# Optimization experiments

Hardware: AMD Instinct MI355X
Metric: run time of the kernel (lower is better)

Reference implementation:

```python
import jax, jax.numpy as jnp
import numpy as np

NUM_SLOTS = 8
DIM = 256
ITERS = 3
EPS_LN = 1e-5

def _ln(x, g, b):
    mu = jnp.mean(x, axis=-1, keepdims=True)
    var = jnp.var(x, axis=-1, keepdims=True)
    return (x - mu) * jax.lax.rsqrt(var + EPS_LN) * g + b

def setup_inputs() -> dict:
    key = jax.random.key(0)
    ks = jax.random.split(key, 16)
    d = DIM
    s = 1.0 / np.sqrt(d)
    inp = {
        'x': jax.random.normal(ks[0], (64, 4096, d), jnp.float32),
        'noise': jax.random.normal(ks[1], (64, NUM_SLOTS, d), jnp.float32),
        'slots_mu': jax.random.normal(ks[2], (1, 1, d), jnp.float32),
        'slots_logsigma': jnp.zeros((1, 1, d), jnp.float32),
        'Wq': jax.random.uniform(ks[3], (d, d), jnp.float32, -s, s),
        'Wk': jax.random.uniform(ks[4], (d, d), jnp.float32, -s, s),
        'Wv': jax.random.uniform(ks[5], (d, d), jnp.float32, -s, s),
        'W_ih': jax.random.uniform(ks[6], (3 * d, d), jnp.float32, -s, s),
        'W_hh': jax.random.uniform(ks[7], (3 * d, d), jnp.float32, -s, s),
        'b_ih': jax.random.uniform(ks[8], (3 * d,), jnp.float32, -s, s),
        'b_hh': jax.random.uniform(ks[9], (3 * d,), jnp.float32, -s, s),
        'W1': jax.random.uniform(ks[10], (d, d), jnp.float32, -s, s),
        'b1': jax.random.uniform(ks[11], (d,), jnp.float32, -s, s),
        'W2': jax.random.uniform(ks[12], (d, d), jnp.float32, -s, s),
        'b2': jax.random.uniform(ks[13], (d,), jnp.float32, -s, s),
        'g_in': jnp.ones((d,), jnp.float32), 'be_in': jnp.zeros((d,), jnp.float32),
        'g_sl': jnp.ones((d,), jnp.float32), 'be_sl': jnp.zeros((d,), jnp.float32),
        'g_ff': jnp.ones((d,), jnp.float32), 'be_ff': jnp.zeros((d,), jnp.float32),
    }
    return inp

def _gru(x, h, W_ih, W_hh, b_ih, b_hh):
    # torch.nn.GRUCell math; x,h: [M, d]
    gi = x @ W_ih.T + b_ih
    gh = h @ W_hh.T + b_hh
    i_r, i_z, i_n = jnp.split(gi, 3, axis=-1)
    h_r, h_z, h_n = jnp.split(gh, 3, axis=-1)
    r = jax.nn.sigmoid(i_r + h_r)
    z = jax.nn.sigmoid(i_z + h_z)
    n = jnp.tanh(i_n + r * h_n)
    return (1.0 - z) * n + z * h

def reference(x, noise, slots_mu, slots_logsigma, Wq, Wk, Wv, W_ih, W_hh, b_ih, b_hh,
              W1, b1, W2, b2, g_in, be_in, g_sl, be_sl, g_ff, be_ff):
    B, N, d = x.shape
    scale = d ** (-0.5)
    x = _ln(x, g_in, be_in)
    slots = slots_mu + noise * jnp.exp(slots_logsigma)  # [B, K, d]
    # k/v are loop-invariant; hoist (same math as original)
    k = jnp.einsum('bnd,ed->bne', x, Wk)
    v = jnp.einsum('bnd,ed->bne', x, Wv)
    for _ in range(ITERS):
        slots_prev = slots
        q = jnp.einsum('bkd,ed->bke', _ln(slots, g_sl, be_sl), Wq)
        attn = jax.nn.softmax(jnp.einsum('bkd,bnd->bkn', q, k) * scale, axis=-1) + 1e-8
        attn = attn / jnp.sum(attn, axis=-1, keepdims=True)
        updates = jnp.einsum('bkn,bnd->bkd', attn, v)
        slots = _gru(updates.reshape(-1, d), slots_prev.reshape(-1, d),
                     W_ih, W_hh, b_ih, b_hh).reshape(B, NUM_SLOTS, d)
        h = jax.nn.relu(jnp.einsum('bkd,ed->bke', _ln(slots, g_ff, be_ff), W1) + b1)
        slots = slots + jnp.einsum('bkd,ed->bke', h, W2) + b2
    return slots.reshape(B, NUM_SLOTS * d)
```

## Files before the change

### kernel.cpp

```cpp
#include <hip/hip_runtime.h>
#include <cstddef>

#define DIM 256
#define NSLOT 8
#define BATCH 64
#define NTOK 4096
#define SEGB 16
#define NPART SEGB
#define ITERS 3
#define EPS 1e-5f

typedef short bf16x8 __attribute__((ext_vector_type(8)));
typedef short bf16x4 __attribute__((ext_vector_type(4)));
typedef float f32x4  __attribute__((ext_vector_type(4)));

static __device__ __forceinline__ short f2bf(float f) {
    union { float f; unsigned u; } v; v.f = f;
    unsigned r = v.u + 0x7fffu + ((v.u >> 16) & 1u);
    return (short)(r >> 16);
}

enum : size_t {
    OFF_M     = 0,
    OFF_WIHT  = OFF_M    + 256 * 256,
    OFF_WHHT  = OFF_WIHT + 256 * 768,
    OFF_WVT   = OFF_WHHT + 256 * 768,
    OFF_W1T   = OFF_WVT  + 256 * 256,
    OFF_W2T   = OFF_W1T  + 256 * 256,
    OFF_SLOTS = OFF_W2T  + 256 * 256,
    OFF_SNEW  = OFF_SLOTS + BATCH * NSLOT * 256,
    OFF_QT    = OFF_SNEW  + BATCH * NSLOT * 256,
    OFF_H     = OFF_QT    + BATCH * NSLOT * 256,
    OFF_UPD   = OFF_H     + BATCH * NSLOT * 256,
    OFF_UPART = OFF_UPD   + BATCH * NSLOT * 256,
    OFF_LPART = OFF_UPART + (size_t)BATCH * NPART * NSLOT * 256,
    WS_FLOATS = OFF_LPART + BATCH * NPART * 16
};

__global__ __launch_bounds__(256) void k_transpose(const float* __restrict__ w_ih,
                                                   const float* __restrict__ w_hh,
                                                   const float* __restrict__ wv,
                                                   const float* __restrict__ w1,
                                                   const float* __restrict__ w2,
                                                   float* __restrict__ ws) {
    int z = blockIdx.z;
    const float* src;
    float* dst;
    int R;
    if (z == 0)      { src = w_ih; dst = ws + OFF_WIHT; R = 768; }
    else if (z == 1) { src = w_hh; dst = ws + OFF_WHHT; R = 768; }
    else if (z == 2) { src = wv;   dst = ws + OFF_WVT;  R = 256; }
    else if (z == 3) { src = w1;   dst = ws + OFF_W1T;  R = 256; }
    else             { src = w2;   dst = ws + OFF_W2T;  R = 256; }
    if ((int)blockIdx.x * 32 >= R) return;
    __shared__ float tile[32][33];
    int lx = threadIdx.x & 31, ly = threadIdx.x >> 5;
    int r0 = blockIdx.x * 32, c0 = blockIdx.y * 32;
#pragma unroll
    for (int p = 0; p < 4; ++p)
        tile[ly + p * 8][lx] = src[(size_t)(r0 + ly + p * 8) * 256 + c0 + lx];
    __syncthreads();
#pragma unroll
    for (int p = 0; p < 4; ++p)
        dst[(size_t)(c0 + ly + p * 8) * R + r0 + lx] = tile[lx][ly + p * 8];
}

__global__ __launch_bounds__(256) void k_m(const float* __restrict__ wq,
                                           const float* __restrict__ wk,
                                           float* __restrict__ ws) {
    int d = blockIdx.x, t = threadIdx.x;
    float acc = 0.f;
    for (int e = 0; e < 256; ++e)
        acc += wq[e * 256 + d] * wk[e * 256 + t];
    ws[OFF_M + d * 256 + t] = acc * 0.0625f;
}

__global__ __launch_bounds__(256) void k_init(const float* __restrict__ mu,
                                              const float* __restrict__ logsig,
                                              const float* __restrict__ noise,
                                              float* __restrict__ ws) {
    int i = blockIdx.x * 256 + threadIdx.x;
    int d = i & 255;
    ws[OFF_SLOTS + i] = mu[d] + noise[i] * __expf(logsig[d]);
}

__global__ __launch_bounds__(256) void k_qt(float* __restrict__ ws,
                                            const float* __restrict__ g_sl,
                                            const float* __restrict__ be_sl) {
    __shared__ float ln[2048];
    int chunk = blockIdx.x, b = blockIdx.y;
    int t = threadIdx.x, wave = t >> 6, lane = t & 63;
    const float* slots = ws + OFF_SLOTS + b * 2048;
    float4 gf = ((const float4*)g_sl)[lane];
    float4 bf = ((const float4*)be_sl)[lane];
#pragma unroll
    for (int rr = 0; rr < 2; ++rr) {
        int r = wave + rr * 4;
        float4 v = ((const float4*)(slots + r * 256))[lane];
        float s1 = v.x + v.y + v.z + v.w;
        float s2 = v.x * v.x + v.y * v.y + v.z * v.z + v.w * v.w;
#pragma unroll
        for (int m = 1; m < 64; m <<= 1) { s1 += __shfl_xor(s1, m); s2 += __shfl_xor(s2, m); }
        float mu = s1 * (1.f / 256.f);
        float rstd = rsqrtf(s2 * (1.f / 256.f) - mu * mu + EPS);
        float4 o;
        o.x = (v.x - mu) * rstd * gf.x + bf.x;
        o.y = (v.y - mu) * rstd * gf.y + bf.y;
        o.z = (v.z - mu) * rstd * gf.z + bf.z;
        o.w = (v.w - mu) * rstd * gf.w + bf.w;
        *((float4*)&ln[r * 256 + lane * 4]) = o;
    }
    __syncthreads();
    const float* M = ws + OFF_M;
    int k0 = t >> 6;
    int e = chunk * 64 + (t & 63);
    float a0 = 0.f, a1 = 0.f;
    for (int d = 0; d < 256; ++d) {
        float m = M[d * 256 + e];
        a0 += ln[k0 * 256 + d] * m;
        a1 += ln[(k0 + 4) * 256 + d] * m;
    }
    float* qt = ws + OFF_QT + b * 2048;
    qt[k0 * 256 + e] = a0;
    qt[(k0 + 4) * 256 + e] = a1;
}

__global__ __launch_bounds__(256) void k_attn(const float* __restrict__ x,
                                              const float* __restrict__ g_in,
                                              const float* __restrict__ be_in,
                                              float* __restrict__ ws) {
    int seg = blockIdx.x, b = blockIdx.y;
    int t = threadIdx.x;
    int w = t >> 6, lane = t & 63;
    int q = lane >> 4, s16 = lane & 15;

    __shared__ short qhi[16 * 264];
    __shared__ short xT[256 * 64];
    __shared__ short Etmp[16 * 72];
    __shared__ float GsL[16], CsL[16];
    __shared__ float lsum[4][8], b1sLDS[4][8];

    const float* qtg = ws + OFF_QT + b * 2048;

    for (int idx = t; idx < 16 * 264; idx += 256) {
        int s = idx / 264, d = idx - s * 264;
        float v = (s < 8 && d < 256) ? qtg[s * 256 + d] * g_in[d] : 0.f;
        qhi[idx] = f2bf(v);
    }
    {
        if (t >= 8 && t < 16) { GsL[t] = 0.f; CsL[t] = 0.f; }
        int s = t >> 5, j = t & 31;
        float pg = 0.f, pc = 0.f;
        for (int d = j; d < 256; d += 32) {
            float qv = qtg[s * 256 + d];
            pg += qv * g_in[d];
            pc += qv * be_in[d];
        }
#pragma unroll
        for (int m = 1; m < 32; m <<= 1) { pg += __shfl_xor(pg, m); pc += __shfl_xor(pc, m); }
        if (j == 0) { GsL[s] = pg; CsL[s] = pc; }
    }
    __syncthreads();

    bf16x8 qf[8];
#pragma unroll
    for (int i = 0; i < 8; ++i)
        qf[i] = *(const bf16x8*)&qhi[s16 * 264 + i * 32 + q * 8];

    float Gv = GsL[s16], Cv = CsL[s16];

    f32x4 U[4];
#pragma unroll
    for (int c = 0; c < 4; ++c) U[c] = (f32x4){0.f, 0.f, 0.f, 0.f};
    float lacc = 0.f, b1acc = 0.f;

    const int tokens_per_block = NTOK / SEGB;
    const int tiles = tokens_per_block / 64;
    int mytok_base = seg * tokens_per_block + w * 16 + s16;
    int g0 = ((w * 16 + s16) >> 3);
    int t7 = s16 & 7;

    for (int tt = 0; tt < tiles; ++tt) {
        const float* xr = x + ((size_t)b * NTOK + (size_t)(mytok_base + tt * 64)) * 256 + q * 8;
        const float4* xp = (const float4*)xr;
        float4 xa[8], xb[8];
#pragma unroll
        for (int i = 0; i < 8; ++i) { xa[i] = xp[8 * i]; xb[i] = xp[8 * i + 1]; }
        float s1 = 0.f, s2 = 0.f;
#pragma unroll
        for (int i = 0; i < 8; ++i) {
            s1 += xa[i].x + xa[i].y + xa[i].z + xa[i].w + xb[i].x + xb[i].y + xb[i].z + xb[i].w;
            s2 += xa[i].x * xa[i].x + xa[i].y * xa[i].y + xa[i].z * xa[i].z + xa[i].w * xa[i].w
                + xb[i].x * xb[i].x + xb[i].y * xb[i].y + xb[i].z * xb[i].z + xb[i].w * xb[i].w;
        }
        s1 += __shfl_xor(s1, 16); s2 += __shfl_xor(s2, 16);
        s1 += __shfl_xor(s1, 32); s2 += __shfl_xor(s2, 32);
        float mu = s1 * (1.f / 256.f);
        float rstd = rsqrtf(s2 * (1.f / 256.f) - mu * mu + EPS);

        bf16x8 af[8];
#pragma unroll
        for (int i = 0; i < 8; ++i) {
            bf16x8 f;
            f[0] = f2bf(xa[i].x); f[1] = f2bf(xa[i].y); f[2] = f2bf(xa[i].z); f[3] = f2bf(xa[i].w);
            f[4] = f2bf(xb[i].x); f[5] = f2bf(xb[i].y); f[6] = f2bf(xb[i].z); f[7] = f2bf(xb[i].w);
            af[i] = f;
        }

        f32x4 Lc = (f32x4){0.f, 0.f, 0.f, 0.f};
#pragma unroll
        for (int i = 0; i < 8; ++i)
            Lc = __builtin_amdgcn_mfma_f32_16x16x32_bf16(af[i], qf[i], Lc, 0, 0, 0);

        float mur[4], rsr[4];
#pragma unroll
        for (int r = 0; r < 4; ++r) {
            mur[r] = __shfl(mu, q * 4 + r);
            rsr[r] = __shfl(rstd, q * 4 + r);
        }
        bf16x4 e2;
#pragma unroll
        for (int r = 0; r < 4; ++r) {
            float logit = rsr[r] * Lc[r] - mur[r] * rsr[r] * Gv + Cv;
            float E = __expf(fminf(logit, 30.f));
            lacc += E;
            b1acc += E * mur[r] * rsr[r];
            e2[r] = f2bf(E * rsr[r]);
        }

        __syncthreads();

#pragma unroll
        for (int i = 0; i < 8; ++i) {
            int Ki = (4 * i + q) & 7;
            int dbase = i * 32 + q * 8;
            bf16x8 f = af[i];
#pragma unroll
            for (int e = 0; e < 8; ++e) {
                int gp = (g0 ^ e ^ Ki) & 7;
                xT[((dbase + e) << 6) + (gp << 3) + t7] = f[e];
            }
        }
        *(bf16x4*)&Etmp[s16 * 72 + w * 16 + q * 4] = e2;

        __syncthreads();

        bf16x8 ea0 = *(const bf16x8*)&Etmp[s16 * 72 + q * 8];
        bf16x8 ea1 = *(const bf16x8*)&Etmp[s16 * 72 + 32 + q * 8];
#pragma unroll
        for (int c = 0; c < 4; ++c) {
            int d = (4 * w + c) * 16 + s16;
            int swz = (d ^ (d >> 3)) & 7;
            const short* row = &xT[d << 6];
            bf16x8 b0 = *(const bf16x8*)&row[((q ^ swz) & 7) << 3];
            bf16x8 b1 = *(const bf16x8*)&row[(((4 + q) ^ swz) & 7) << 3];
            U[c] = __builtin_amdgcn_mfma_f32_16x16x32_bf16(ea0, b0, U[c], 0, 0, 0);
            U[c] = __builtin_amdgcn_mfma_f32_16x16x32_bf16(ea1, b1, U[c], 0, 0, 0);
        }
    }

    lacc += __shfl_xor(lacc, 16); lacc += __shfl_xor(lacc, 32);
    b1acc += __shfl_xor(b1acc, 16); b1acc += __shfl_xor(b1acc, 32);
    __syncthreads();
    if (q == 0 && s16 < 8) { lsum[w][s16] = lacc; b1sLDS[w][s16] = b1acc; }
    __syncthreads();
    float* lpart = ws + OFF_LPART + (size_t)(b * NPART + seg) * 16;
    if (t < 8)  lpart[t] = lsum[0][t] + lsum[1][t] + lsum[2][t] + lsum[3][t];
    if (t >= 8 && t < 16) {
        int s = t - 8;
        lpart[8 + s] = b1sLDS[0][s] + b1sLDS[1][s] + b1sLDS[2][s] + b1sLDS[3][s];
    }
    float* up = ws + OFF_UPART + (size_t)(b * NPART + seg) * NSLOT * 256;
#pragma unroll
    for (int c = 0; c < 4; ++c) {
        int d = (4 * w + c) * 16 + s16;
#pragma unroll
        for (int r = 0; r < 4; ++r) {
            int slot = q * 4 + r;
            if (slot < 8) up[slot * 256 + d] = U[c][r];
        }
    }
}

__global__ __launch_bounds__(256) void k_upd(float* __restrict__ ws,
                                             const float* __restrict__ g_in,
                                             const float* __restrict__ be_in) {
    __shared__ float uc[2048];
    __shared__ float lsv[8], b1v[8];
    int b = blockIdx.x, t = threadIdx.x;
    if (t < 8) {
        float ls = 0.f, b1 = 0.f;
        for (int g = 0; g < NPART; ++g) {
            ls += ws[OFF_LPART + (size_t)(b * NPART + g) * 16 + t];
            b1 += ws[OFF_LPART + (size_t)(b * NPART + g) * 16 + 8 + t];
        }
        lsv[t] = ls; b1v[t] = b1;
    }
    float acc[8] = {0.f, 0.f, 0.f, 0.f, 0.f, 0.f, 0.f, 0.f};
    const float* up0 = ws + OFF_UPART + (size_t)b * NPART * 8 * 256;
    for (int g = 0; g < NPART; ++g) {
        const float* up = up0 + g * 2048;
#pragma unroll
        for (int s = 0; s < 8; ++s) acc[s] += up[s * 256 + t];
    }
    __syncthreads();
    float gd = g_in[t], bd = be_in[t];
#pragma unroll
    for (int s = 0; s < 8; ++s) {
        uc[s * 256 + t] = (gd * (acc[s] - b1v[s]) + bd * lsv[s]) / lsv[s];
    }
    __syncthreads();
    const float* WvT = ws + OFF_WVT;
    int k0 = t >> 6;
    int e0 = t & 63;
    float o0[4] = {0.f, 0.f, 0.f, 0.f};
    float o1[4] = {0.f, 0.f, 0.f, 0.f};
    for (int d = 0; d < 256; ++d) {
        float u0 = uc[k0 * 256 + d], u1 = uc[(k0 + 4) * 256 + d];
#pragma unroll
        for (int c = 0; c < 4; ++c) {
            float w = WvT[d * 256 + c * 64 + e0];
            o0[c] += u0 * w;
            o1[c] += u1 * w;
        }
    }
    float* updg = ws + OFF_UPD + b * 2048;
#pragma unroll
    for (int c = 0; c < 4; ++c) {
        updg[k0 * 256 + c * 64 + e0] = o0[c];
        updg[(k0 + 4) * 256 + c * 64 + e0] = o1[c];
    }
}

__global__ __launch_bounds__(256) void k_gru(float* __restrict__ ws,
                                             const float* __restrict__ b_ih,
                                             const float* __restrict__ b_hh) {
    __shared__ float upd[2048], sl[2048];
    int cg = blockIdx.x, b = blockIdx.y, t = threadIdx.x;
    const float* updg = ws + OFF_UPD + b * 2048;
    const float* slg = ws + OFF_SLOTS + b * 2048;
#pragma unroll
    for (int j = 0; j < 8; ++j) {
        upd[j * 256 + t] = updg[j * 256 + t];
        sl[j * 256 + t] = slg[j * 256 + t];
    }
    __syncthreads();
    int k = t >> 5, j = t & 31, c = cg * 32 + j;
    const float* WihT = ws + OFF_WIHT;
    const float* WhhT = ws + OFF_WHHT;
    float ar = 0.f, az = 0.f, an = 0.f, hr = 0.f, hz = 0.f, hn = 0.f;
    for (int d = 0; d < 256; ++d) {
        float ud = upd[k * 256 + d], sd = sl[k * 256 + d];
        const float* wi = WihT + d * 768;
        const float* wh = WhhT + d * 768;
        ar += ud * wi[c];       az += ud * wi[256 + c]; an += ud * wi[512 + c];
        hr += sd * wh[c];       hz += sd * wh[256 + c]; hn += sd * wh[512 + c];
    }
    float rg = 1.f / (1.f + __expf(-(ar + b_ih[c] + hr + b_hh[c])));
    float zg = 1.f / (1.f + __expf(-(az + b_ih[256 + c] + hz + b_hh[256 + c])));
    float ng = tanhf(an + b_ih[512 + c] + rg * (hn + b_hh[512 + c]));
    float hval = sl[k * 256 + c];
    ws[OFF_SNEW + b * 2048 + k * 256 + c] = (1.f - zg) * ng + zg * hval;
}

__global__ __launch_bounds__(256) void k_mlp1(float* __restrict__ ws,
                                              const float* __restrict__ g_ff,
                                              const float* __restrict__ be_ff,
                                              const float* __restrict__ b1v) {
    __shared__ float ln[2048];
    int chunk = blockIdx.x, b = blockIdx.y;
    int t = threadIdx.x, wave = t >> 6, lane = t & 63;
    const float* sn = ws + OFF_SNEW + b * 2048;
    float4 gf = ((const float4*)g_ff)[lane];
    float4 bf = ((const float4*)be_ff)[lane];
#pragma unroll
    for (int rr = 0; rr < 2; ++rr) {
        int r = wave + rr * 4;
        float4 v = ((const float4*)(sn + r * 256))[lane];
        float s1 = v.x + v.y + v.z + v.w;
        float s2 = v.x * v.x + v.y * v.y + v.z * v.z + v.w * v.w;
#pragma unroll
        for (int m = 1; m < 64; m <<= 1) { s1 += __shfl_xor(s1, m); s2 += __shfl_xor(s2, m); }
        float mu = s1 * (1.f / 256.f);
        float rstd = rsqrtf(s2 * (1.f / 256.f) - mu * mu + EPS);
        float4 o;
        o.x = (v.x - mu) * rstd * gf.x + bf.x;
        o.y = (v.y - mu) * rstd * gf.y + bf.y;
        o.z = (v.z - mu) * rstd * gf.z + bf.z;
        o.w = (v.w - mu) * rstd * gf.w + bf.w;
        *((float4*)&ln[r * 256 + lane * 4]) = o;
    }
    __syncthreads();
    const float* W1T = ws + OFF_W1T;
    int k0 = t >> 6, e = chunk * 64 + (t & 63);
    float a0 = 0.f, a1 = 0.f;
    for (int d = 0; d < 256; ++d) {
        float w = W1T[d * 256 + e];
        a0 += ln[k0 * 256 + d] * w;
        a1 += ln[(k0 + 4) * 256 + d] * w;
    }
    float* h = ws + OFF_H + b * 2048;
    float bb = b1v[e];
    h[k0 * 256 + e] = fmaxf(a0 + bb, 0.f);
    h[(k0 + 4) * 256 + e] = fmaxf(a1 + bb, 0.f);
}

__global__ __launch_bounds__(256) void k_mlp2(float* __restrict__ ws,
                                              const float* __restrict__ b2v,
                                              float* __restrict__ dout) {
    __shared__ float hl[2048];
    int chunk = blockIdx.x, b = blockIdx.y, t = threadIdx.x;
    const float* h = ws + OFF_H + b * 2048;
#pragma unroll
    for (int j = 0; j < 8; ++j) hl[j * 256 + t] = h[j * 256 + t];
    __syncthreads();
    int k0 = t >> 6, e = chunk * 64 + (t & 63);
    const float* W2T = ws + OFF_W2T;
    float a0 = 0.f, a1 = 0.f;
    for (int d = 0; d < 256; ++d) {
        float w = W2T[d * 256 + e];
        a0 += hl[k0 * 256 + d] * w;
        a1 += hl[(k0 + 4) * 256 + d] * w;
    }
    const float* sn = ws + OFF_SNEW + b * 2048;
    float bb = b2v[e];
    float out0 = sn[k0 * 256 + e] + a0 + bb;
    float out1 = sn[(k0 + 4) * 256 + e] + a1 + bb;
    float* sl = ws + OFF_SLOTS + b * 2048;
    sl[k0 * 256 + e] = out0;
    sl[(k0 + 4) * 256 + e] = out1;
    if (dout) {
        dout[b * 2048 + k0 * 256 + e] = out0;
        dout[b * 2048 + (k0 + 4) * 256 + e] = out1;
    }
}

extern "C" void kernel_launch(void* const* d_in, const int* in_sizes, int n_in,
                              void* d_out, int out_size, void* d_ws, size_t ws_size,
                              hipStream_t stream) {
    const float* x      = (const float*)d_in[0];
    const float* noise  = (const float*)d_in[1];
    const float* mu     = (const float*)d_in[2];
    const float* logsig = (const float*)d_in[3];
    const float* Wq     = (const float*)d_in[4];
    const float* Wk     = (const float*)d_in[5];
    const float* Wv     = (const float*)d_in[6];
    const float* W_ih   = (const float*)d_in[7];
    const float* W_hh   = (const float*)d_in[8];
    const float* b_ih   = (const float*)d_in[9];
    const float* b_hh   = (const float*)d_in[10];
    const float* W1     = (const float*)d_in[11];
    const float* b1     = (const float*)d_in[12];
    const float* W2     = (const float*)d_in[13];
    const float* b2     = (const float*)d_in[14];
    const float* g_in   = (const float*)d_in[15];
    const float* be_in  = (const float*)d_in[16];
    const float* g_sl   = (const float*)d_in[17];
    const float* be_sl  = (const float*)d_in[18];
    const float* g_ff   = (const float*)d_in[19];
    const float* be_ff  = (const float*)d_in[20];
    float* ws = (float*)d_ws;
    float* out = (float*)d_out;

    hipLaunchKernelGGL(k_transpose, dim3(24, 8, 5), dim3(256), 0, stream, W_ih, W_hh, Wv, W1, W2, ws);
    hipLaunchKernelGGL(k_m, dim3(256), dim3(256), 0, stream, Wq, Wk, ws);
    hipLaunchKernelGGL(k_init, dim3(512), dim3(256), 0, stream, mu, logsig, noise, ws);
    for (int it = 0; it < ITERS; ++it) {
        hipLaunchKernelGGL(k_qt, dim3(4, 64), dim3(256), 0, stream, ws, g_sl, be_sl);
        hipLaunchKernelGGL(k_attn, dim3(SEGB, 64), dim3(256), 0, stream, x, g_in, be_in, ws);
        hipLaunchKernelGGL(k_upd, dim3(64), dim3(256), 0, stream, ws, g_in, be_in);
        hipLaunchKernelGGL(k_gru, dim3(8, 64), dim3(256), 0, stream, ws, b_ih, b_hh);
        hipLaunchKernelGGL(k_mlp1, dim3(4, 64), dim3(256), 0, stream, ws, g_ff, be_ff, b1);
        hipLaunchKernelGGL(k_mlp2, dim3(4, 64), dim3(256), 0, stream, ws, b2,
                           (it == ITERS - 1) ? out : nullptr);
    }
}
```

Measured before the change: 905.6 us.

## Fuse slot update, GRU, MLP and next-iteration query into one kernel

Replaces the per-iteration k_upd, k_gru, k_mlp1, k_mlp2 and k_qt launches with a single kernel in which each block handles two slots of one batch and keeps intermediates in shared memory. The next iteration's query projection (LN plus M matmul) is folded into the tail of the fused kernel, so k_qt runs only once before the loop. This removes several launches and global round-trips per iteration. In exchange each block redoes weight reads for only two slots, which lowers weight reuse, and the upd stage now runs on 256 blocks instead of 64.

```diff
diff --git a/kernel.cpp b/kernel.cpp
--- a/kernel.cpp
+++ b/kernel.cpp
@@ -282,156 +282,127 @@
     }
 }
 
-__global__ __launch_bounds__(256) void k_upd(float* __restrict__ ws,
-                                             const float* __restrict__ g_in,
-                                             const float* __restrict__ be_in) {
-    __shared__ float uc[2048];
-    __shared__ float lsv[8], b1v[8];
-    int b = blockIdx.x, t = threadIdx.x;
-    if (t < 8) {
-        float ls = 0.f, b1 = 0.f;
-        for (int g = 0; g < NPART; ++g) {
-            ls += ws[OFF_LPART + (size_t)(b * NPART + g) * 16 + t];
-            b1 += ws[OFF_LPART + (size_t)(b * NPART + g) * 16 + 8 + t];
-        }
-        lsv[t] = ls; b1v[t] = b1;
-    }
-    float acc[8] = {0.f, 0.f, 0.f, 0.f, 0.f, 0.f, 0.f, 0.f};
-    const float* up0 = ws + OFF_UPART + (size_t)b * NPART * 8 * 256;
-    for (int g = 0; g < NPART; ++g) {
-        const float* up = up0 + g * 2048;
-#pragma unroll
-        for (int s = 0; s < 8; ++s) acc[s] += up[s * 256 + t];
-    }
-    __syncthreads();
-    float gd = g_in[t], bd = be_in[t];
-#pragma unroll
-    for (int s = 0; s < 8; ++s) {
-        uc[s * 256 + t] = (gd * (acc[s] - b1v[s]) + bd * lsv[s]) / lsv[s];
-    }
-    __syncthreads();
-    const float* WvT = ws + OFF_WVT;
-    int k0 = t >> 6;
-    int e0 = t & 63;
-    float o0[4] = {0.f, 0.f, 0.f, 0.f};
-    float o1[4] = {0.f, 0.f, 0.f, 0.f};
-    for (int d = 0; d < 256; ++d) {
-        float u0 = uc[k0 * 256 + d], u1 = uc[(k0 + 4) * 256 + d];
-#pragma unroll
-        for (int c = 0; c < 4; ++c) {
-            float w = WvT[d * 256 + c * 64 + e0];
-            o0[c] += u0 * w;
-            o1[c] += u1 * w;
-        }
-    }
-    float* updg = ws + OFF_UPD + b * 2048;
-#pragma unroll
-    for (int c = 0; c < 4; ++c) {
-        updg[k0 * 256 + c * 64 + e0] = o0[c];
-        updg[(k0 + 4) * 256 + c * 64 + e0] = o1[c];
-    }
-}
-
-__global__ __launch_bounds__(256) void k_gru(float* __restrict__ ws,
-                                             const float* __restrict__ b_ih,
-                                             const float* __restrict__ b_hh) {
-    __shared__ float upd[2048], sl[2048];
-    int cg = blockIdx.x, b = blockIdx.y, t = threadIdx.x;
-    const float* updg = ws + OFF_UPD + b * 2048;
-    const float* slg = ws + OFF_SLOTS + b * 2048;
-#pragma unroll
-    for (int j = 0; j < 8; ++j) {
-        upd[j * 256 + t] = updg[j * 256 + t];
-        sl[j * 256 + t] = slg[j * 256 + t];
-    }
-    __syncthreads();
-    int k = t >> 5, j = t & 31, c = cg * 32 + j;
-    const float* WihT = ws + OFF_WIHT;
-    const float* WhhT = ws + OFF_WHHT;
-    float ar = 0.f, az = 0.f, an = 0.f, hr = 0.f, hz = 0.f, hn = 0.f;
-    for (int d = 0; d < 256; ++d) {
-        float ud = upd[k * 256 + d], sd = sl[k * 256 + d];
-        const float* wi = WihT + d * 768;
-        const float* wh = WhhT + d * 768;
-        ar += ud * wi[c];       az += ud * wi[256 + c]; an += ud * wi[512 + c];
-        hr += sd * wh[c];       hz += sd * wh[256 + c]; hn += sd * wh[512 + c];
-    }
-    float rg = 1.f / (1.f + __expf(-(ar + b_ih[c] + hr + b_hh[c])));
-    float zg = 1.f / (1.f + __expf(-(az + b_ih[256 + c] + hz + b_hh[256 + c])));
-    float ng = tanhf(an + b_ih[512 + c] + rg * (hn + b_hh[512 + c]));
-    float hval = sl[k * 256 + c];
-    ws[OFF_SNEW + b * 2048 + k * 256 + c] = (1.f - zg) * ng + zg * hval;
-}
-
-__global__ __launch_bounds__(256) void k_mlp1(float* __restrict__ ws,
-                                              const float* __restrict__ g_ff,
-                                              const float* __restrict__ be_ff,
-                                              const float* __restrict__ b1v) {
-    __shared__ float ln[2048];
-    int chunk = blockIdx.x, b = blockIdx.y;
-    int t = threadIdx.x, wave = t >> 6, lane = t & 63;
-    const float* sn = ws + OFF_SNEW + b * 2048;
-    float4 gf = ((const float4*)g_ff)[lane];
-    float4 bf = ((const float4*)be_ff)[lane];
-#pragma unroll
-    for (int rr = 0; rr < 2; ++rr) {
-        int r = wave + rr * 4;
-        float4 v = ((const float4*)(sn + r * 256))[lane];
+static __device__ __forceinline__ void ln_row2(const float* src, float* dst,
+                                               const float* __restrict__ g,
+                                               const float* __restrict__ be,
+                                               int wave, int lane) {
+    if (wave < 2) {
+        float4 v = *(const float4*)(src + wave * 256 + lane * 4);
         float s1 = v.x + v.y + v.z + v.w;
         float s2 = v.x * v.x + v.y * v.y + v.z * v.z + v.w * v.w;
 #pragma unroll
         for (int m = 1; m < 64; m <<= 1) { s1 += __shfl_xor(s1, m); s2 += __shfl_xor(s2, m); }
         float mu = s1 * (1.f / 256.f);
         float rstd = rsqrtf(s2 * (1.f / 256.f) - mu * mu + EPS);
+        float4 gf = ((const float4*)g)[lane];
+        float4 bf = ((const float4*)be)[lane];
         float4 o;
         o.x = (v.x - mu) * rstd * gf.x + bf.x;
         o.y = (v.y - mu) * rstd * gf.y + bf.y;
         o.z = (v.z - mu) * rstd * gf.z + bf.z;
         o.w = (v.w - mu) * rstd * gf.w + bf.w;
-        *((float4*)&ln[r * 256 + lane * 4]) = o;
-    }
-    __syncthreads();
-    const float* W1T = ws + OFF_W1T;
-    int k0 = t >> 6, e = chunk * 64 + (t & 63);
-    float a0 = 0.f, a1 = 0.f;
-    for (int d = 0; d < 256; ++d) {
-        float w = W1T[d * 256 + e];
-        a0 += ln[k0 * 256 + d] * w;
-        a1 += ln[(k0 + 4) * 256 + d] * w;
-    }
-    float* h = ws + OFF_H + b * 2048;
-    float bb = b1v[e];
-    h[k0 * 256 + e] = fmaxf(a0 + bb, 0.f);
-    h[(k0 + 4) * 256 + e] = fmaxf(a1 + bb, 0.f);
-}
-
-__global__ __launch_bounds__(256) void k_mlp2(float* __restrict__ ws,
-                                              const float* __restrict__ b2v,
-                                              float* __restrict__ dout) {
-    __shared__ float hl[2048];
-    int chunk = blockIdx.x, b = blockIdx.y, t = threadIdx.x;
-    const float* h = ws + OFF_H + b * 2048;
-#pragma unroll
-    for (int j = 0; j < 8; ++j) hl[j * 256 + t] = h[j * 256 + t];
-    __syncthreads();
-    int k0 = t >> 6, e = chunk * 64 + (t & 63);
-    const float* W2T = ws + OFF_W2T;
-    float a0 = 0.f, a1 = 0.f;
-    for (int d = 0; d < 256; ++d) {
-        float w = W2T[d * 256 + e];
-        a0 += hl[k0 * 256 + d] * w;
-        a1 += hl[(k0 + 4) * 256 + d] * w;
-    }
-    const float* sn = ws + OFF_SNEW + b * 2048;
-    float bb = b2v[e];
-    float out0 = sn[k0 * 256 + e] + a0 + bb;
-    float out1 = sn[(k0 + 4) * 256 + e] + a1 + bb;
-    float* sl = ws + OFF_SLOTS + b * 2048;
-    sl[k0 * 256 + e] = out0;
-    sl[(k0 + 4) * 256 + e] = out1;
-    if (dout) {
-        dout[b * 2048 + k0 * 256 + e] = out0;
-        dout[b * 2048 + (k0 + 4) * 256 + e] = out1;
+        *(float4*)(dst + wave * 256 + lane * 4) = o;
+    }
+}
+
+__global__ __launch_bounds__(512) void k_fused(float* __restrict__ ws,
+                                               const float* __restrict__ g_in,
+                                               const float* __restrict__ be_in,
+                                               const float* __restrict__ b_ih,
+                                               const float* __restrict__ b_hh,
+                                               const float* __restrict__ g_ff,
+                                               const float* __restrict__ be_ff,
+                                               const float* __restrict__ b1p,
+                                               const float* __restrict__ b2p,
+                                               const float* __restrict__ g_sl,
+                                               const float* __restrict__ be_sl,
+                                               float* __restrict__ dout) {
+    __shared__ __align__(16) float uc[2][256], upd[2][256], sl[2][256], snew[2][256];
+    __shared__ __align__(16) float lnb[2][256], hbuf[2][256], so[2][256];
+    __shared__ float lsv[2], b1vs[2];
+
+    int sp = blockIdx.x, b = blockIdx.y, t = threadIdx.x;
+    int s0 = sp * 2;
+    int s = t >> 8, d = t & 255;
+    int wave = t >> 6, lane = t & 63;
+
+    if (t < 32) {
+        int ss = t >> 4, g = t & 15;
+        const float* lp = ws + OFF_LPART + (size_t)(b * NPART + g) * 16;
+        float lv = lp[s0 + ss];
+        float bv = lp[8 + s0 + ss];
+#pragma unroll
+        for (int m = 1; m < 16; m <<= 1) { lv += __shfl_xor(lv, m); bv += __shfl_xor(bv, m); }
+        if ((t & 15) == 0) { lsv[ss] = lv; b1vs[ss] = bv; }
+    }
+
+    const float* up0 = ws + OFF_UPART + (size_t)b * NPART * NSLOT * 256 + (s0 + s) * 256 + d;
+    float acc = 0.f;
+#pragma unroll
+    for (int g = 0; g < NPART; ++g) acc += up0[(size_t)g * NSLOT * 256];
+    sl[s][d] = ws[OFF_SLOTS + (size_t)b * 2048 + (s0 + s) * 256 + d];
+    __syncthreads();
+    {
+        float gd = g_in[d], bd = be_in[d];
+        uc[s][d] = (gd * (acc - b1vs[s]) + bd * lsv[s]) / lsv[s];
+    }
+    __syncthreads();
+
+    {
+        const float* WvT = ws + OFF_WVT;
+        float o = 0.f;
+        for (int dd = 0; dd < 256; ++dd) o += uc[s][dd] * WvT[dd * 256 + d];
+        upd[s][d] = o;
+    }
+    __syncthreads();
+
+    {
+        const float* WihT = ws + OFF_WIHT;
+        const float* WhhT = ws + OFF_WHHT;
+        float ar = 0.f, az = 0.f, an = 0.f, hr = 0.f, hz = 0.f, hn = 0.f;
+        for (int dd = 0; dd < 256; ++dd) {
+            float ud = upd[s][dd], sd = sl[s][dd];
+            const float* wi = WihT + dd * 768;
+            const float* wh = WhhT + dd * 768;
+            ar += ud * wi[d];       az += ud * wi[256 + d]; an += ud * wi[512 + d];
+            hr += sd * wh[d];       hz += sd * wh[256 + d]; hn += sd * wh[512 + d];
+        }
+        float rg = 1.f / (1.f + __expf(-(ar + b_ih[d] + hr + b_hh[d])));
+        float zg = 1.f / (1.f + __expf(-(az + b_ih[256 + d] + hz + b_hh[256 + d])));
+        float ng = tanhf(an + b_ih[512 + d] + rg * (hn + b_hh[512 + d]));
+        snew[s][d] = (1.f - zg) * ng + zg * sl[s][d];
+    }
+    __syncthreads();
+
+    ln_row2(&snew[0][0], &lnb[0][0], g_ff, be_ff, wave, lane);
+    __syncthreads();
+
+    {
+        const float* W1T = ws + OFF_W1T;
+        float o = 0.f;
+        for (int dd = 0; dd < 256; ++dd) o += lnb[s][dd] * W1T[dd * 256 + d];
+        hbuf[s][d] = fmaxf(o + b1p[d], 0.f);
+    }
+    __syncthreads();
+
+    {
+        const float* W2T = ws + OFF_W2T;
+        float o = 0.f;
+        for (int dd = 0; dd < 256; ++dd) o += hbuf[s][dd] * W2T[dd * 256 + d];
+        float r = snew[s][d] + o + b2p[d];
+        so[s][d] = r;
+        ws[OFF_SLOTS + (size_t)b * 2048 + (s0 + s) * 256 + d] = r;
+        if (dout) dout[(size_t)b * 2048 + (s0 + s) * 256 + d] = r;
+    }
+
+    if (!dout) {
+        __syncthreads();
+        ln_row2(&so[0][0], &lnb[0][0], g_sl, be_sl, wave, lane);
+        __syncthreads();
+        const float* M = ws + OFF_M;
+        float o = 0.f;
+        for (int dd = 0; dd < 256; ++dd) o += lnb[s][dd] * M[dd * 256 + d];
+        ws[OFF_QT + (size_t)b * 2048 + (s0 + s) * 256 + d] = o;
     }
 }
 
@@ -465,13 +436,11 @@
     hipLaunchKernelGGL(k_transpose, dim3(24, 8, 5), dim3(256), 0, stream, W_ih, W_hh, Wv, W1, W2, ws);
     hipLaunchKernelGGL(k_m, dim3(256), dim3(256), 0, stream, Wq, Wk, ws);
     hipLaunchKernelGGL(k_init, dim3(512), dim3(256), 0, stream, mu, logsig, noise, ws);
+    hipLaunchKernelGGL(k_qt, dim3(4, 64), dim3(256), 0, stream, ws, g_sl, be_sl);
     for (int it = 0; it < ITERS; ++it) {
-        hipLaunchKernelGGL(k_qt, dim3(4, 64), dim3(256), 0, stream, ws, g_sl, be_sl);
         hipLaunchKernelGGL(k_attn, dim3(SEGB, 64), dim3(256), 0, stream, x, g_in, be_in, ws);
-        hipLaunchKernelGGL(k_upd, dim3(64), dim3(256), 0, stream, ws, g_in, be_in);
-        hipLaunchKernelGGL(k_gru, dim3(8, 64), dim3(256), 0, stream, ws, b_ih, b_hh);
-        hipLaunchKernelGGL(k_mlp1, dim3(4, 64), dim3(256), 0, stream, ws, g_ff, be_ff, b1);
-        hipLaunchKernelGGL(k_mlp2, dim3(4, 64), dim3(256), 0, stream, ws, b2,
+        hipLaunchKernelGGL(k_fused, dim3(4, 64), dim3(512), 0, stream, ws, g_in, be_in,
+                           b_ih, b_hh, g_ff, be_ff, b1, b2, g_sl, be_sl,
                            (it == ITERS - 1) ? out : nullptr);
     }
 }
```

After: 764.9 us. -15.5%, faster.
